# Kernel tuning notes

Hardware: AMD Instinct MI355X
Metric: run time of the kernel (lower is better)

Reference implementation:

```python
import jax, jax.numpy as jnp
import numpy as np


def setup_inputs() -> dict:
    key = jax.random.key(0)
    k1, k2 = jax.random.split(key)
    x = jax.random.normal(k1, (8, 2048, 1024), dtype=jnp.float32)
    mask = jax.random.randint(k2, (8, 2048), 0, 2, dtype=jnp.int32)
    return {"x": x, "mask": mask}


def reference(x, mask):
    # x: [B, S, D], mask: [B, S] (0 = masked-out key)
    score = jnp.einsum('bqd,bkd->bqk', x, x)                     # [B, S, S]
    score = jnp.where(mask[:, None, :] == 0, -jnp.inf, score)    # mask keys
    attn = jax.nn.softmax(score, axis=2)                         # over keys
    context = jnp.einsum('bqk,bkd->bqd', attn, x)                # [B, S, D]
    return jnp.concatenate(
        [x, context, x + context, x - context, x * context], axis=-1
    )  # [B, S, 5D]
```

## Files before the change

### kernel.cpp

```cpp
#include <hip/hip_runtime.h>
#include <hip/hip_bf16.h>


typedef __attribute__((ext_vector_type(8))) _Float16 half8;
typedef __attribute__((ext_vector_type(8))) unsigned short ushort8;
typedef __attribute__((ext_vector_type(4))) float f32x4;

#define SEQ 2048
#define DIM 1024
#define NBATCH 8
#define BK 32

__device__ __forceinline__ unsigned short f2h(float f) {
  union { _Float16 h; unsigned short u; } cv;
  cv.h = (_Float16)f;
  return cv.u;
}
__device__ __forceinline__ float h2f(unsigned short u) {
  union { _Float16 h; unsigned short u; } cv;
  cv.u = u;
  return (float)cv.h;
}

__device__ __forceinline__ void load16(const void* g, void* l) {
  __builtin_amdgcn_global_load_lds(
      (const __attribute__((address_space(1))) unsigned int*)g,
      (__attribute__((address_space(3))) unsigned int*)l, 16, 0, 0);
}

__global__ __launch_bounds__(256) void k_prep(
    const float* __restrict__ x, unsigned short* __restrict__ xh,
    unsigned short* __restrict__ xT) {
  __shared__ unsigned short tile[32][33];
  int b = blockIdx.z;
  int s0 = blockIdx.x * 32;
  int d0 = blockIdx.y * 32;
  int t = threadIdx.x;
  int r = t >> 3;
  int c4 = (t & 7) * 4;

  long src = (long)(b * SEQ + s0 + r) * DIM + d0 + c4;
  float4 v = *(const float4*)(x + src);
  float vv[4] = {v.x, v.y, v.z, v.w};
  unsigned short hu[4];
#pragma unroll
  for (int j = 0; j < 4; ++j) {
    hu[j] = f2h(vv[j]);
    tile[r][c4 + j] = hu[j];
  }
  *(ushort4*)(xh + src) = make_ushort4(hu[0], hu[1], hu[2], hu[3]);
  __syncthreads();
  unsigned short tv[4];
#pragma unroll
  for (int j = 0; j < 4; ++j) tv[j] = tile[c4 + j][r];
  long dst = (long)(b * DIM + d0 + r) * SEQ + s0 + c4;
  *(ushort4*)(xT + dst) = make_ushort4(tv[0], tv[1], tv[2], tv[3]);
}

#define COMPUTE_TILE(ARR_A, ARR_B, BUF)                                     \
  {                                                                         \
    half8 af[4], bg[4];                                                     \
    _Pragma("unroll") for (int m = 0; m < 4; ++m) {                         \
      int R = wr * 64 + m * 16 + l15;                                       \
      af[m] = *(const half8*)&ARR_A[BUF][R * BK + ((lhi ^ ((R >> 1) & 3)) * 8)]; \
    }                                                                       \
    _Pragma("unroll") for (int n = 0; n < 4; ++n) {                         \
      int R = wc * 64 + n * 16 + l15;                                       \
      bg[n] = *(const half8*)&ARR_B[BUF][R * BK + ((lhi ^ ((R >> 1) & 3)) * 8)]; \
    }                                                                       \
    _Pragma("unroll") for (int m = 0; m < 4; ++m)                           \
      _Pragma("unroll") for (int n = 0; n < 4; ++n)                         \
        acc[m][n] = __builtin_amdgcn_mfma_f32_16x16x32_f16(af[m], bg[n], acc[m][n], 0, 0, 0); \
  }

#define NT_SC 32
__global__ __launch_bounds__(256) void k_scores(
    const unsigned short* __restrict__ xh, unsigned short* __restrict__ S) {
  __shared__ unsigned short As[3][128 * BK];
  __shared__ unsigned short Bs[3][128 * BK];
  int p = blockIdx.x + 136 * blockIdx.z;
  int b = p & 7;
  int t = p >> 3;
  int bm = 0, rem = 16;
  while (t >= rem) { t -= rem; ++bm; --rem; }
  int bn = bm + t;
  int m0 = bm * 128;
  int n0 = bn * 128;
  const unsigned short* xh_b = xh + (long)b * SEQ * DIM;
  unsigned short* S_b = S + (long)b * SEQ * SEQ;

  int tid = threadIdx.x;
  int w = tid >> 6, lane = tid & 63;
  int wr = w >> 1, wc = w & 1;
  int l15 = lane & 15, lhi = lane >> 4;

  int cbase0 = w * 64, cbase1 = 256 + w * 64;
  int c0 = cbase0 + lane, c1 = cbase1 + lane;
  int row0 = c0 >> 2, row1 = c1 >> 2;
  long aoff0 = (long)(m0 + row0) * DIM + ((c0 & 3) ^ ((row0 >> 1) & 3)) * 8;
  long aoff1 = (long)(m0 + row1) * DIM + ((c1 & 3) ^ ((row1 >> 1) & 3)) * 8;
  long boff0 = (long)(n0 + row0) * DIM + ((c0 & 3) ^ ((row0 >> 1) & 3)) * 8;
  long boff1 = (long)(n0 + row1) * DIM + ((c1 & 3) ^ ((row1 >> 1) & 3)) * 8;

#define STAGE_SC(KT, BUF)                                                   \
  {                                                                         \
    int kk_ = (KT) * BK;                                                    \
    load16(xh_b + aoff0 + kk_, &As[BUF][cbase0 * 8]);                       \
    load16(xh_b + aoff1 + kk_, &As[BUF][cbase1 * 8]);                       \
    load16(xh_b + boff0 + kk_, &Bs[BUF][cbase0 * 8]);                       \
    load16(xh_b + boff1 + kk_, &Bs[BUF][cbase1 * 8]);                       \
  }

  f32x4 acc[4][4];
#pragma unroll
  for (int m = 0; m < 4; ++m)
#pragma unroll
    for (int n = 0; n < 4; ++n)
#pragma unroll
      for (int j = 0; j < 4; ++j) acc[m][n][j] = 0.0f;

  STAGE_SC(0, 0);
  STAGE_SC(1, 1);
  STAGE_SC(2, 2);
  int cur = 0;
  for (int kt = 0; kt < NT_SC - 2; ++kt) {
    asm volatile("s_waitcnt vmcnt(8)" ::: "memory");
    __builtin_amdgcn_s_barrier();
    __builtin_amdgcn_sched_barrier(0);
    COMPUTE_TILE(As, Bs, cur);
    __builtin_amdgcn_sched_barrier(0);
    __builtin_amdgcn_s_barrier();
    if (kt + 3 < NT_SC) STAGE_SC(kt + 3, cur);
    cur = (cur == 2) ? 0 : cur + 1;
  }
  asm volatile("s_waitcnt vmcnt(4)" ::: "memory");
  __builtin_amdgcn_s_barrier();
  COMPUTE_TILE(As, Bs, (NT_SC - 2) % 3);
  asm volatile("s_waitcnt vmcnt(0)" ::: "memory");
  __builtin_amdgcn_s_barrier();
  COMPUTE_TILE(As, Bs, (NT_SC - 1) % 3);

#pragma unroll
  for (int m = 0; m < 4; ++m)
#pragma unroll
    for (int n = 0; n < 4; ++n)
#pragma unroll
      for (int j = 0; j < 4; ++j) {
        int r = m0 + wr * 64 + m * 16 + lhi * 4 + j;
        int c = n0 + wc * 64 + n * 16 + l15;
        S_b[(long)r * SEQ + c] = f2h(acc[m][n][j]);
      }
  if (bm != bn) {
#pragma unroll
    for (int m = 0; m < 4; ++m)
#pragma unroll
      for (int n = 0; n < 4; ++n) {
        int r0 = m0 + wr * 64 + m * 16 + lhi * 4;
        int c = n0 + wc * 64 + n * 16 + l15;
        *(ushort4*)&S_b[(long)c * SEQ + r0] = make_ushort4(
            f2h(acc[m][n][0]), f2h(acc[m][n][1]),
            f2h(acc[m][n][2]), f2h(acc[m][n][3]));
      }
  }
}

__global__ __launch_bounds__(256) void k_softmax(
    const unsigned short* __restrict__ S, const int* __restrict__ mask,
    unsigned short* __restrict__ P) {
  int w = threadIdx.x >> 6, lane = threadIdx.x & 63;
  long row = (long)blockIdx.x * 4 + w;
  int b = (int)(row >> 11);
  const unsigned short* Sp = S + row * SEQ;
  const int* mp = mask + b * SEQ;
  unsigned short* Pp = P + row * SEQ;

  float sv[32];
  float mx = -__builtin_inff();
#pragma unroll
  for (int ci = 0; ci < 4; ++ci) {
    int col = ci * 512 + lane * 8;
    ushort8 v = *(const ushort8*)(Sp + col);
    int4 ma = *(const int4*)(mp + col);
    int4 mb = *(const int4*)(mp + col + 4);
    int mk[8] = {ma.x, ma.y, ma.z, ma.w, mb.x, mb.y, mb.z, mb.w};
#pragma unroll
    for (int j = 0; j < 8; ++j) {
      float s = mk[j] ? h2f(v[j]) : -__builtin_inff();
      sv[ci * 8 + j] = s;
      mx = fmaxf(mx, s);
    }
  }
#pragma unroll
  for (int off = 32; off; off >>= 1) mx = fmaxf(mx, __shfl_xor(mx, off));
  float pv[32];
  float sum = 0.0f;
#pragma unroll
  for (int i = 0; i < 32; ++i) {
    pv[i] = expf(sv[i] - mx);
    sum += pv[i];
  }
#pragma unroll
  for (int off = 32; off; off >>= 1) sum += __shfl_xor(sum, off);
  float inv = 1.0f / sum;
#pragma unroll
  for (int ci = 0; ci < 4; ++ci) {
    int col = ci * 512 + lane * 8;
    ushort8 o;
#pragma unroll
    for (int j = 0; j < 8; ++j) o[j] = f2h(pv[ci * 8 + j] * inv);
    *(ushort8*)(Pp + col) = o;
  }
}

#define NT_CTX 32
__global__ __launch_bounds__(512, 2) void k_context(
    const unsigned short* __restrict__ P, const unsigned short* __restrict__ xT,
    const float* __restrict__ x, float* __restrict__ out) {
  __shared__ unsigned short As[2 * 16384];
  __shared__ unsigned short Bs[2 * 16384];
  int p = blockIdx.x;
  int b = p & 7;
  int q = p >> 3;
  int n0 = (q & 3) * 256;
  int m0 = (q >> 2) * 256;
  const unsigned short* A_b = P + (long)b * SEQ * SEQ;
  const unsigned short* B_b = xT + (long)b * DIM * SEQ;

  int tid = threadIdx.x;
  int w = tid >> 6, lane = tid & 63;
  int wr = w >> 2, wc = w & 3;
  int l15 = lane & 15, lhi = lane >> 4;

  int c0 = w * 128 + lane, c1 = w * 128 + 64 + lane;
  int R0 = c0 >> 2, R1 = c1 >> 2;
  int sw0 = ((c0 & 3) ^ ((R0 >> 1) & 3)) * 8;
  int sw1 = ((c1 & 3) ^ ((R1 >> 1) & 3)) * 8;
  const unsigned short* PA0 = A_b + (long)(m0 + R0) * SEQ + sw0;
  const unsigned short* PA1 = A_b + (long)(m0 + R1) * SEQ + sw1;
  const unsigned short* PB0 = B_b + (long)(n0 + R0) * SEQ + sw0;
  const unsigned short* PB1 = B_b + (long)(n0 + R1) * SEQ + sw1;
  int ldg0 = (w * 128) * 8;
  int ldg1 = (w * 128 + 64) * 8;

#define STG_A(KT, KK, BUF)                                              \
  {                                                                     \
    load16(PA0 + (KT) * 64 + (KK) * 32, &As[(BUF)*16384 + (KK)*8192 + ldg0]); \
    load16(PA1 + (KT) * 64 + (KK) * 32, &As[(BUF)*16384 + (KK)*8192 + ldg1]); \
  }
#define STG_B(KT, KK, BUF)                                              \
  {                                                                     \
    load16(PB0 + (KT) * 64 + (KK) * 32, &Bs[(BUF)*16384 + (KK)*8192 + ldg0]); \
    load16(PB1 + (KT) * 64 + (KK) * 32, &Bs[(BUF)*16384 + (KK)*8192 + ldg1]); \
  }

  int swr = (lhi ^ ((l15 >> 1) & 3)) * 8;
  int arow = (wr * 128 + l15) * 32;
  int brow = (wc * 64 + l15) * 32;

#define PHASE_CTX(BUF, KK, DO_STG_A, DO_STG_B, STKT, STKK, STBUF)             \
  {                                                                           \
    half8 af[8], bg[4];                                                       \
    _Pragma("unroll") for (int n = 0; n < 4; ++n)                             \
        bg[n] = *(const half8*)&Bs[(BUF)*16384 + (KK)*8192 + brow + n * 512 + swr]; \
    _Pragma("unroll") for (int m = 0; m < 8; ++m)                             \
        af[m] = *(const half8*)&As[(BUF)*16384 + (KK)*8192 + arow + m * 512 + swr]; \
    if (DO_STG_A) STG_A(STKT, STKK, STBUF);                                   \
    if (DO_STG_B) STG_B(STKT, STKK, STBUF);                                   \
    __builtin_amdgcn_s_barrier();                                             \
    asm volatile("s_waitcnt lgkmcnt(0)" ::: "memory");                        \
    __builtin_amdgcn_sched_barrier(0);                                        \
    __builtin_amdgcn_s_setprio(1);                                            \
    _Pragma("unroll") for (int m = 0; m < 8; ++m)                             \
      _Pragma("unroll") for (int n = 0; n < 4; ++n)                           \
        acc[m][n] = __builtin_amdgcn_mfma_f32_16x16x32_f16(                   \
            bg[n], af[m], acc[m][n], 0, 0, 0);                                \
    __builtin_amdgcn_s_setprio(0);                                            \
    __builtin_amdgcn_sched_barrier(0);                                        \
  }

  f32x4 acc[8][4];
#pragma unroll
  for (int m = 0; m < 8; ++m)
#pragma unroll
    for (int n = 0; n < 4; ++n)
#pragma unroll
      for (int j = 0; j < 4; ++j) acc[m][n][j] = 0.0f;

  STG_A(0, 0, 0); STG_B(0, 0, 0);
  STG_A(0, 1, 0); STG_B(0, 1, 0);
  STG_A(1, 0, 1); STG_B(1, 0, 1);
  asm volatile("s_waitcnt vmcnt(4)" ::: "memory");
  __builtin_amdgcn_s_barrier();

  for (int kt = 0; kt < NT_CTX; ++kt) {
    int c = kt & 1, o = c ^ 1;
    int haveN1 = (kt + 1 < NT_CTX), haveN2 = (kt + 2 < NT_CTX);
    PHASE_CTX(c, 0, haveN1, haveN1, kt + 1, 1, o);
    __builtin_amdgcn_s_barrier();
    PHASE_CTX(c, 1, haveN2, haveN2, kt + 2, 0, c);
    if (kt < NT_CTX - 2) {
      asm volatile("s_waitcnt vmcnt(4)" ::: "memory");
    } else if (kt == NT_CTX - 2) {
      asm volatile("s_waitcnt vmcnt(0)" ::: "memory");
    }
    __builtin_amdgcn_s_barrier();
  }

  const float* x_b = x + (long)b * SEQ * DIM;
  float* out_b = out + (long)b * SEQ * (5 * DIM);
#pragma unroll
  for (int m = 0; m < 8; ++m)
#pragma unroll
    for (int n = 0; n < 4; ++n) {
      int qi = m0 + wr * 128 + m * 16 + l15;
      int d = n0 + wc * 64 + n * 16 + lhi * 4;
      f32x4 c4 = acc[m][n];
      f32x4 xv = *(const f32x4*)&x_b[(long)qi * DIM + d];
      long base = (long)qi * (5 * DIM) + d;
      __builtin_nontemporal_store(xv,       (f32x4*)&out_b[base]);
      __builtin_nontemporal_store(c4,       (f32x4*)&out_b[base + DIM]);
      __builtin_nontemporal_store(xv + c4,  (f32x4*)&out_b[base + 2 * DIM]);
      __builtin_nontemporal_store(xv - c4,  (f32x4*)&out_b[base + 3 * DIM]);
      __builtin_nontemporal_store(xv * c4,  (f32x4*)&out_b[base + 4 * DIM]);
    }
}

extern "C" void kernel_launch(void* const* d_in, const int* in_sizes, int n_in,
                              void* d_out, int out_size, void* d_ws, size_t ws_size,
                              hipStream_t stream) {
  const float* x = (const float*)d_in[0];
  const int* mask = (const int*)d_in[1];
  float* out = (float*)d_out;
  char* ws = (char*)d_ws;

  const size_t HB = (size_t)NBATCH * SEQ * DIM * 2;
  unsigned short* xh = (unsigned short*)ws;
  unsigned short* xT = (unsigned short*)(ws + HB);
  unsigned short* P = (unsigned short*)(ws + 2 * HB);
  const size_t PB = (size_t)NBATCH * SEQ * SEQ * 2;
  const size_t SB = (size_t)NBATCH * SEQ * SEQ * 2;
  unsigned short* S;
  if (ws_size >= 2 * HB + PB + SB) {
    S = (unsigned short*)(ws + 2 * HB + PB);
  } else {
    S = (unsigned short*)d_out;
  }

  k_prep<<<dim3(SEQ / 32, DIM / 32, NBATCH), 256, 0, stream>>>(x, xh, xT);
  k_scores<<<dim3(136, 1, NBATCH), 256, 0, stream>>>(xh, S);
  k_softmax<<<NBATCH * SEQ / 4, 256, 0, stream>>>(S, mask, P);
  k_context<<<dim3(256, 1, 1), 512, 0, stream>>>(P, xT, x, out);
}
```

Before: 250.8 us.

## Compact unmasked keys so the context GEMM skips masked-out columns

Adds a per-batch prefix scan over the mask that builds a list of kept key indices. The transposed fp16 x is gathered only for those keys, and softmax writes probabilities scattered into compacted column positions, zero-padded to a multiple of 64. The context GEMM then loops only over the compacted K tiles, which removes roughly the masked share of its MFMA work and loads. It adds two small kernels, uncoalesced 2-byte scattered stores in softmax, and nontemporal stores for the score matrix.

```diff
diff --git a/kernel.cpp b/kernel.cpp
--- a/kernel.cpp
+++ b/kernel.cpp
@@ -4,6 +4,7 @@
 
 typedef __attribute__((ext_vector_type(8))) _Float16 half8;
 typedef __attribute__((ext_vector_type(8))) unsigned short ushort8;
+typedef __attribute__((ext_vector_type(4))) unsigned short us4;
 typedef __attribute__((ext_vector_type(4))) float f32x4;
 
 #define SEQ 2048
@@ -29,32 +30,84 @@
 }
 
 __global__ __launch_bounds__(256) void k_prep(
-    const float* __restrict__ x, unsigned short* __restrict__ xh,
-    unsigned short* __restrict__ xT) {
-  __shared__ unsigned short tile[32][33];
+    const float* __restrict__ x, unsigned short* __restrict__ xh) {
+  long i = ((long)blockIdx.x * 256 + threadIdx.x) * 8;
+  float4 a = *(const float4*)(x + i);
+  float4 c = *(const float4*)(x + i + 4);
+  ushort8 o;
+  o[0] = f2h(a.x); o[1] = f2h(a.y); o[2] = f2h(a.z); o[3] = f2h(a.w);
+  o[4] = f2h(c.x); o[5] = f2h(c.y); o[6] = f2h(c.z); o[7] = f2h(c.w);
+  *(ushort8*)(xh + i) = o;
+}
+
+__global__ __launch_bounds__(64) void k_scan(
+    const int* __restrict__ mask, int* __restrict__ cidx,
+    int* __restrict__ orig, int* __restrict__ meta) {
+  int b = blockIdx.x, lane = threadIdx.x;
+  const int* mp = mask + b * SEQ;
+  int loc[32];
+  int cnt = 0;
+#pragma unroll
+  for (int i = 0; i < 8; ++i) {
+    int4 v = *(const int4*)(mp + lane * 32 + i * 4);
+    loc[i * 4 + 0] = v.x; loc[i * 4 + 1] = v.y;
+    loc[i * 4 + 2] = v.z; loc[i * 4 + 3] = v.w;
+    cnt += (v.x != 0) + (v.y != 0) + (v.z != 0) + (v.w != 0);
+  }
+  int incl = cnt;
+#pragma unroll
+  for (int off = 1; off < 64; off <<= 1) {
+    int t = __shfl_up(incl, off, 64);
+    if (lane >= off) incl += t;
+  }
+  int run = incl - cnt;
+  int* cb = cidx + b * SEQ;
+  int* ob = orig + b * SEQ;
+#pragma unroll
+  for (int i = 0; i < 32; ++i) {
+    int col = lane * 32 + i;
+    cb[col] = run;
+    if (loc[i]) { ob[run] = col; ++run; }
+  }
+  if (lane == 63) {
+    int nb = incl;
+    int nt = (nb + 63) >> 6;
+    if (nt < 2) nt = 2;
+    meta[b] = nb;
+    meta[8 + b] = nt;
+  }
+}
+
+__global__ __launch_bounds__(256) void k_gatherT(
+    const unsigned short* __restrict__ xh, const int* __restrict__ orig,
+    const int* __restrict__ meta, unsigned short* __restrict__ xTc) {
   int b = blockIdx.z;
-  int s0 = blockIdx.x * 32;
-  int d0 = blockIdx.y * 32;
-  int t = threadIdx.x;
-  int r = t >> 3;
-  int c4 = (t & 7) * 4;
-
-  long src = (long)(b * SEQ + s0 + r) * DIM + d0 + c4;
-  float4 v = *(const float4*)(x + src);
-  float vv[4] = {v.x, v.y, v.z, v.w};
-  unsigned short hu[4];
-#pragma unroll
-  for (int j = 0; j < 4; ++j) {
-    hu[j] = f2h(vv[j]);
-    tile[r][c4 + j] = hu[j];
-  }
-  *(ushort4*)(xh + src) = make_ushort4(hu[0], hu[1], hu[2], hu[3]);
+  int j0 = blockIdx.x * 64;
+  int d0 = blockIdx.y * 64;
+  int nb = meta[b];
+  int npad = meta[8 + b] * 64;
+  if (j0 >= npad) return;
+  __shared__ unsigned short t[64][72];
+  int r = threadIdx.x >> 2;
+  int c0 = (threadIdx.x & 3) * 16;
+  int j = j0 + r;
+  ushort8 v0 = {0, 0, 0, 0, 0, 0, 0, 0};
+  ushort8 v1 = {0, 0, 0, 0, 0, 0, 0, 0};
+  if (j < nb) {
+    int src = orig[b * SEQ + j];
+    const unsigned short* sp = xh + ((long)b * SEQ + src) * DIM + d0 + c0;
+    v0 = *(const ushort8*)sp;
+    v1 = *(const ushort8*)(sp + 8);
+  }
+  *(ushort8*)&t[r][c0] = v0;
+  *(ushort8*)&t[r][c0 + 8] = v1;
   __syncthreads();
-  unsigned short tv[4];
-#pragma unroll
-  for (int j = 0; j < 4; ++j) tv[j] = tile[c4 + j][r];
-  long dst = (long)(b * DIM + d0 + r) * SEQ + s0 + c4;
-  *(ushort4*)(xT + dst) = make_ushort4(tv[0], tv[1], tv[2], tv[3]);
+  ushort8 w0, w1;
+#pragma unroll
+  for (int k = 0; k < 8; ++k) { w0[k] = t[c0 + k][r]; w1[k] = t[c0 + 8 + k][r]; }
+  unsigned short* dp = xTc + ((long)b * DIM + d0 + r) * SEQ + j0 + c0;
+  *(ushort8*)dp = w0;
+  *(ushort8*)(dp + 8) = w1;
 }
 
 #define COMPUTE_TILE(ARR_A, ARR_B, BUF)                                     \
@@ -148,7 +201,7 @@
       for (int j = 0; j < 4; ++j) {
         int r = m0 + wr * 64 + m * 16 + lhi * 4 + j;
         int c = n0 + wc * 64 + n * 16 + l15;
-        S_b[(long)r * SEQ + c] = f2h(acc[m][n][j]);
+        __builtin_nontemporal_store(f2h(acc[m][n][j]), &S_b[(long)r * SEQ + c]);
       }
   if (bm != bn) {
 #pragma unroll
@@ -157,15 +210,16 @@
       for (int n = 0; n < 4; ++n) {
         int r0 = m0 + wr * 64 + m * 16 + lhi * 4;
         int c = n0 + wc * 64 + n * 16 + l15;
-        *(ushort4*)&S_b[(long)c * SEQ + r0] = make_ushort4(
-            f2h(acc[m][n][0]), f2h(acc[m][n][1]),
-            f2h(acc[m][n][2]), f2h(acc[m][n][3]));
+        us4 pk = {f2h(acc[m][n][0]), f2h(acc[m][n][1]),
+                  f2h(acc[m][n][2]), f2h(acc[m][n][3])};
+        __builtin_nontemporal_store(pk, (us4*)&S_b[(long)c * SEQ + r0]);
       }
   }
 }
 
 __global__ __launch_bounds__(256) void k_softmax(
     const unsigned short* __restrict__ S, const int* __restrict__ mask,
+    const int* __restrict__ cidx, const int* __restrict__ meta,
     unsigned short* __restrict__ P) {
   int w = threadIdx.x >> 6, lane = threadIdx.x & 63;
   long row = (long)blockIdx.x * 4 + w;
@@ -202,20 +256,26 @@
 #pragma unroll
   for (int off = 32; off; off >>= 1) sum += __shfl_xor(sum, off);
   float inv = 1.0f / sum;
+  const int* cb = cidx + b * SEQ;
 #pragma unroll
   for (int ci = 0; ci < 4; ++ci) {
     int col = ci * 512 + lane * 8;
-    ushort8 o;
-#pragma unroll
-    for (int j = 0; j < 8; ++j) o[j] = f2h(pv[ci * 8 + j] * inv);
-    *(ushort8*)(Pp + col) = o;
-  }
-}
-
-#define NT_CTX 32
+    int4 ca = *(const int4*)(cb + col);
+    int4 c2 = *(const int4*)(cb + col + 4);
+    int cd[8] = {ca.x, ca.y, ca.z, ca.w, c2.x, c2.y, c2.z, c2.w};
+#pragma unroll
+    for (int j = 0; j < 8; ++j)
+      if (sv[ci * 8 + j] > -1e30f) Pp[cd[j]] = f2h(pv[ci * 8 + j] * inv);
+  }
+  int nb = meta[b];
+  int npad = meta[8 + b] * 64;
+  for (int j = nb + lane; j < npad; j += 64) Pp[j] = 0;
+}
+
 __global__ __launch_bounds__(512, 2) void k_context(
     const unsigned short* __restrict__ P, const unsigned short* __restrict__ xT,
-    const float* __restrict__ x, float* __restrict__ out) {
+    const float* __restrict__ x, const int* __restrict__ meta,
+    float* __restrict__ out) {
   __shared__ unsigned short As[2 * 16384];
   __shared__ unsigned short Bs[2 * 16384];
   int p = blockIdx.x;
@@ -223,6 +283,7 @@
   int q = p >> 3;
   int n0 = (q & 3) * 256;
   int m0 = (q >> 2) * 256;
+  int nt = meta[8 + b];
   const unsigned short* A_b = P + (long)b * SEQ * SEQ;
   const unsigned short* B_b = xT + (long)b * DIM * SEQ;
 
@@ -292,15 +353,15 @@
   asm volatile("s_waitcnt vmcnt(4)" ::: "memory");
   __builtin_amdgcn_s_barrier();
 
-  for (int kt = 0; kt < NT_CTX; ++kt) {
+  for (int kt = 0; kt < nt; ++kt) {
     int c = kt & 1, o = c ^ 1;
-    int haveN1 = (kt + 1 < NT_CTX), haveN2 = (kt + 2 < NT_CTX);
+    int haveN1 = (kt + 1 < nt), haveN2 = (kt + 2 < nt);
     PHASE_CTX(c, 0, haveN1, haveN1, kt + 1, 1, o);
     __builtin_amdgcn_s_barrier();
     PHASE_CTX(c, 1, haveN2, haveN2, kt + 2, 0, c);
-    if (kt < NT_CTX - 2) {
+    if (kt < nt - 2) {
       asm volatile("s_waitcnt vmcnt(4)" ::: "memory");
-    } else if (kt == NT_CTX - 2) {
+    } else if (kt == nt - 2) {
       asm volatile("s_waitcnt vmcnt(0)" ::: "memory");
     }
     __builtin_amdgcn_s_barrier();
@@ -334,20 +395,27 @@
   char* ws = (char*)d_ws;
 
   const size_t HB = (size_t)NBATCH * SEQ * DIM * 2;
-  unsigned short* xh = (unsigned short*)ws;
-  unsigned short* xT = (unsigned short*)(ws + HB);
-  unsigned short* P = (unsigned short*)(ws + 2 * HB);
   const size_t PB = (size_t)NBATCH * SEQ * SEQ * 2;
   const size_t SB = (size_t)NBATCH * SEQ * SEQ * 2;
+  const size_t IB = (size_t)NBATCH * SEQ * 4;
+  unsigned short* xh  = (unsigned short*)ws;
+  unsigned short* xTc = (unsigned short*)(ws + HB);
+  unsigned short* Pc  = (unsigned short*)(ws + 2 * HB);
+  int* cidx = (int*)(ws + 2 * HB + PB);
+  int* orig = (int*)(ws + 2 * HB + PB + IB);
+  int* meta = (int*)(ws + 2 * HB + PB + 2 * IB);
+  size_t meta_end = 2 * HB + PB + 2 * IB + 1024;
   unsigned short* S;
-  if (ws_size >= 2 * HB + PB + SB) {
-    S = (unsigned short*)(ws + 2 * HB + PB);
+  if (ws_size >= meta_end + SB) {
+    S = (unsigned short*)(ws + meta_end);
   } else {
     S = (unsigned short*)d_out;
   }
 
-  k_prep<<<dim3(SEQ / 32, DIM / 32, NBATCH), 256, 0, stream>>>(x, xh, xT);
+  k_prep<<<dim3((int)((size_t)NBATCH * SEQ * DIM / (256 * 8)), 1, 1), 256, 0, stream>>>(x, xh);
+  k_scan<<<dim3(NBATCH, 1, 1), 64, 0, stream>>>(mask, cidx, orig, meta);
   k_scores<<<dim3(136, 1, NBATCH), 256, 0, stream>>>(xh, S);
-  k_softmax<<<NBATCH * SEQ / 4, 256, 0, stream>>>(S, mask, P);
-  k_context<<<dim3(256, 1, 1), 512, 0, stream>>>(P, xT, x, out);
-}
+  k_gatherT<<<dim3(32, 16, NBATCH), 256, 0, stream>>>(xh, orig, meta, xTc);
+  k_softmax<<<NBATCH * SEQ / 4, 256, 0, stream>>>(S, mask, cidx, meta, Pc);
+  k_context<<<dim3(256, 1, 1), 512, 0, stream>>>(Pc, xTc, x, meta, out);
+}
```

After: 277.6 us. +10.7%, slower.
